# Kernel optimization log

Hardware: AMD Instinct MI355X
Metric: run time of the kernel (lower is better)

Reference implementation:

```python
import jax, jax.numpy as jnp
import numpy as np

B, D_IN, N_EXP, D_EXP, TOP_K = 8192, 1024, 8, 1024, 2


def setup_inputs() -> dict:
    key = jax.random.key(0)
    ks = jax.random.split(key, 6)
    s_in = 1.0 / np.sqrt(D_IN)
    s_exp = 1.0 / np.sqrt(D_EXP)
    return {
        "x": jax.random.normal(ks[0], (B, D_IN), jnp.float32),
        "gate_w": jax.random.normal(ks[1], (D_IN, N_EXP), jnp.float32) * s_in,
        "w1": jax.random.normal(ks[2], (N_EXP, D_IN, D_EXP), jnp.float32) * s_in,
        "b1": jax.random.normal(ks[3], (N_EXP, D_EXP), jnp.float32) * 0.01,
        "w2": jax.random.normal(ks[4], (N_EXP, D_EXP, D_EXP), jnp.float32) * s_exp,
        "b2": jax.random.normal(ks[5], (N_EXP, D_EXP), jnp.float32) * 0.01,
    }


def _moe(x, gate_w, w1, b1, w2, b2):
    # Gating: top-k sparse softmax over expert logits.
    gate_logits = x @ gate_w                          # (B, E)
    top_vals, top_idx = jax.lax.top_k(gate_logits, TOP_K)  # (B, K)
    # softmax over only the top-k logits == softmax of -inf-scattered logits
    top_w = jax.nn.softmax(top_vals, axis=-1)          # (B, K)
    gate_weights = jnp.zeros_like(gate_logits).at[
        jnp.arange(x.shape[0])[:, None], top_idx
    ].set(top_w)                                       # (B, E)
    # Dense all-expert MLP (matches torch.stack over experts).
    h = jax.nn.gelu(jnp.einsum("bd,edf->ebf", x, w1) + b1[:, None, :],
                    approximate=False)                 # (E, B, F)
    expert_outs = jnp.einsum("ebf,efg->ebg", h, w2) + b2[:, None, :]  # (E, B, G)
    output = jnp.einsum("be,ebg->bg", gate_weights, expert_outs)      # (B, G)
    return output, gate_weights


def reference(x, gate_w, w1, b1, w2, b2):
    return _moe(x, gate_w, w1, b1, w2, b2)
```

## Files before the change

### kernel.cpp

```cpp
#include <hip/hip_runtime.h>
#include <math.h>
#include <stdint.h>


#define NTOK   8192
#define DIN    1024
#define NEXP   8
#define DEXP   1024
#define MAXROWS 17408
#define MAXT   136

typedef __bf16 bf16x8_t __attribute__((ext_vector_type(8)));
typedef float f32x4 __attribute__((ext_vector_type(4)));

__device__ __forceinline__ unsigned short f2bf(float f) {
  union { float f; unsigned int u; } v; v.f = f;
  unsigned int u = v.u;
  u += 0x7fffu + ((u >> 16) & 1u);
  return (unsigned short)(u >> 16);
}

__device__ __forceinline__ float bf2f(unsigned short s) {
  union { unsigned int u; float f; } v; v.u = ((unsigned int)s) << 16;
  return v.f;
}

__device__ __forceinline__ void async16(const void* g, void* l) {
  __builtin_amdgcn_global_load_lds((const __attribute__((address_space(1))) void*)g,
                                   (__attribute__((address_space(3))) void*)l, 16, 0, 0);
}

__device__ __forceinline__ float gelu_fast(float v) {
  float u = v * (1.5957691216057308f + 0.07135481627f * v * v);
  return v * (1.0f / (1.0f + __expf(-u)));
}

__device__ __forceinline__ void transpose_tile(const float* s, unsigned short* d,
                                               float* tile, int tid) {
  int a = tid & 15, r0 = tid >> 4;
  #pragma unroll
  for (int p = 0; p < 4; ++p) {
    int r = r0 + p * 16;
    float4 v = *(const float4*)(s + (size_t)r * 1024 + a * 4);
    tile[r * 65 + a * 4 + 0] = v.x;
    tile[r * 65 + a * 4 + 1] = v.y;
    tile[r * 65 + a * 4 + 2] = v.z;
    tile[r * 65 + a * 4 + 3] = v.w;
  }
  __syncthreads();
  #pragma unroll
  for (int p = 0; p < 4; ++p) {
    int nr = r0 + p * 16;
    ushort4 o;
    o.x = f2bf(tile[(a * 4 + 0) * 65 + nr]);
    o.y = f2bf(tile[(a * 4 + 1) * 65 + nr]);
    o.z = f2bf(tile[(a * 4 + 2) * 65 + nr]);
    o.w = f2bf(tile[(a * 4 + 3) * 65 + nr]);
    *(ushort4*)(d + (size_t)nr * 1024 + a * 4) = o;
  }
}

__global__ __launch_bounds__(256) void prep_kernel(const float* __restrict__ x,
                                                   const float* __restrict__ gw,
                                                   const float* __restrict__ w1,
                                                   const float* __restrict__ w2,
                                                   unsigned short* __restrict__ xbf,
                                                   unsigned short* __restrict__ w1T,
                                                   unsigned short* __restrict__ w2T,
                                                   float* __restrict__ outGate,
                                                   int* __restrict__ topE,
                                                   float* __restrict__ topW,
                                                   int* __restrict__ rowTok) {
  __shared__ __align__(16) char smem[32768];
  int b = blockIdx.x;
  int tid = threadIdx.x;
  if (b >= 6144) {
    int base = (b - 6144) * 1024 + tid * 4;
    *(int4*)(rowTok + base) = make_int4(-1, -1, -1, -1);
    return;
  }
  if (b >= 2048) {
    int idx = b - 2048;
    const float* src = (idx < 2048) ? w1 : w2;
    unsigned short* dst = (idx < 2048) ? w1T : w2T;
    idx &= 2047;
    int e = idx >> 8, rest = idx & 255, kt = rest >> 4, nt = rest & 15;
    const float* s = src + (size_t)e * DIN * DEXP + (size_t)kt * 64 * 1024 + nt * 64;
    unsigned short* d = dst + (size_t)e * DIN * DEXP + (size_t)nt * 64 * 1024 + kt * 64;
    transpose_tile(s, d, (float*)smem, tid);
    return;
  }
  float (*gwT)[1024] = (float(*)[1024])smem;
  #pragma unroll
  for (int it = 0; it < 8; ++it) {
    int idx = it * 256 + tid;
    int fk = idx >> 1;
    int e0 = (idx & 1) * 4;
    float4 g = *(const float4*)(gw + fk * 8 + e0);
    gwT[e0 + 0][fk] = g.x; gwT[e0 + 1][fk] = g.y;
    gwT[e0 + 2][fk] = g.z; gwT[e0 + 3][fk] = g.w;
  }
  __syncthreads();

  int lane = tid & 63, wv = tid >> 6;
  int t = b * 4 + wv;
  const float4* xr = (const float4*)(x + (size_t)t * 1024);
  ushort4* xo = (ushort4*)(xbf + (size_t)t * 1024);
  double acc[NEXP];
  #pragma unroll
  for (int e = 0; e < NEXP; ++e) acc[e] = 0.0;
  #pragma unroll
  for (int j = 0; j < 4; ++j) {
    int q = lane + 64 * j;
    float4 v = xr[q];
    ushort4 r;
    r.x = f2bf(v.x); r.y = f2bf(v.y); r.z = f2bf(v.z); r.w = f2bf(v.w);
    xo[q] = r;
    float vv[4] = {v.x, v.y, v.z, v.w};
    #pragma unroll
    for (int e = 0; e < NEXP; ++e) {
      float4 g = *(const float4*)&gwT[e][4 * q];
      acc[e] += (double)vv[0] * (double)g.x;
      acc[e] += (double)vv[1] * (double)g.y;
      acc[e] += (double)vv[2] * (double)g.z;
      acc[e] += (double)vv[3] * (double)g.w;
    }
  }
  #pragma unroll
  for (int off = 32; off > 0; off >>= 1) {
    #pragma unroll
    for (int e = 0; e < NEXP; ++e) acc[e] += __shfl_xor(acc[e], off);
  }
  if (lane == 0) {
    int e0 = 0; double v0 = acc[0];
    #pragma unroll
    for (int e = 1; e < NEXP; ++e) if (acc[e] > v0) { v0 = acc[e]; e0 = e; }
    int e1 = -1; double v1 = -1e300;
    #pragma unroll
    for (int e = 0; e < NEXP; ++e) if (e != e0 && acc[e] > v1) { v1 = acc[e]; e1 = e; }
    float ex = expf((float)(v1 - v0));
    float inv = 1.0f / (1.0f + ex);
    float w0 = inv, w1v = ex * inv;
    float g8[8];
    #pragma unroll
    for (int e = 0; e < NEXP; ++e) g8[e] = 0.f;
    g8[e0] = w0; g8[e1] = w1v;
    float4* gp = (float4*)(outGate + t * 8);
    gp[0] = *(float4*)&g8[0];
    gp[1] = *(float4*)&g8[4];
    topE[t * 2 + 0] = e0; topE[t * 2 + 1] = e1;
    topW[t * 2 + 0] = w0; topW[t * 2 + 1] = w1v;
  }
}

__global__ __launch_bounds__(1024) void slot_kernel(const int* __restrict__ topE,
                                                    int* __restrict__ topRow,
                                                    int* __restrict__ rowTok,
                                                    int* __restrict__ tileExpert,
                                                    int* __restrict__ tileRowBase) {
  __shared__ int wtot[16][NEXP];
  __shared__ int wbase[16][NEXP];
  __shared__ int soff[NEXP];
  int tid = threadIdx.x;
  int lane = tid & 63, wv = tid >> 6;
  int a0 = tid * 16;
  unsigned long long pk = 0ull;
  int cnt[NEXP];
  #pragma unroll
  for (int e = 0; e < NEXP; ++e) cnt[e] = 0;
  #pragma unroll
  for (int i = 0; i < 4; ++i) {
    int4 ev = *(const int4*)(topE + a0 + i * 4);
    int e4[4] = {ev.x, ev.y, ev.z, ev.w};
    #pragma unroll
    for (int m = 0; m < 4; ++m) {
      int e = e4[m];
      pk |= (unsigned long long)e << ((i * 4 + m) * 4);
      cnt[e]++;
    }
  }
  int excl[NEXP];
  #pragma unroll
  for (int e = 0; e < NEXP; ++e) {
    int v = cnt[e], sum = v;
    #pragma unroll
    for (int d = 1; d < 64; d <<= 1) {
      int u = __shfl_up(sum, d);
      if (lane >= d) sum += u;
    }
    excl[e] = sum - v;
    if (lane == 63) wtot[wv][e] = sum;
  }
  __syncthreads();
  if (tid == 0) {
    int counts[NEXP];
    for (int e = 0; e < NEXP; ++e) {
      int s = 0;
      for (int w = 0; w < 16; ++w) { wbase[w][e] = s; s += wtot[w][e]; }
      counts[e] = s;
    }
    int row = 0, tl = 0;
    for (int e = 0; e < NEXP; ++e) {
      soff[e] = row;
      int nt = (counts[e] + 127) >> 7;
      for (int i = 0; i < nt; ++i) { tileExpert[tl] = e; tileRowBase[tl] = row + i * 128; ++tl; }
      row += nt << 7;
    }
    for (; tl < MAXT; ++tl) tileExpert[tl] = -1;
  }
  __syncthreads();
  int base[NEXP], run[NEXP];
  #pragma unroll
  for (int e = 0; e < NEXP; ++e) { base[e] = soff[e] + wbase[wv][e] + excl[e]; run[e] = 0; }
  for (int i = 0; i < 16; ++i) {
    int e = (int)((pk >> (i * 4)) & 7ull);
    int row = base[e] + run[e]++;
    rowTok[row] = (a0 + i) >> 1;
    topRow[a0 + i] = row;
  }
}

template <bool GATHER, bool GELU>
__device__ __forceinline__ void moe_gemm_body(
    const unsigned short* __restrict__ Asrc,
    const unsigned short* __restrict__ Wt,
    const float* __restrict__ bias,
    const int* __restrict__ tileExpert,
    const int* __restrict__ tileRowBase,
    const int* __restrict__ rowTok,
    unsigned short* __restrict__ Out,
    unsigned short* sm) {
  int e = tileExpert[blockIdx.y];
  if (e < 0) return;
  int rowBase = tileRowBase[blockIdx.y];
  int n0 = blockIdx.x * 128;

  int tid = threadIdx.x;
  int lane = tid & 63, wv = tid >> 6;
  int wr = wv >> 1, wc = wv & 1;

  int p = lane >> 3, pos = lane & 7;
  int L = pos ^ p;
  int rowoff = wv * 16 + p * 2 + (L >> 2);
  int qsw = L & 3;

  int rsel = lane & 15, quad = lane >> 4;
  int prow = rsel >> 1;
  int co = (((rsel & 1) * 4 + quad) ^ prow) * 8 + prow * 64;

  int arow[2];
  #pragma unroll
  for (int j = 0; j < 2; ++j) {
    int r = rowBase + j * 64 + rowoff;
    if (GATHER) { int tk = rowTok[r]; arow[j] = tk < 0 ? 0 : tk; }
    else arow[j] = r;
  }
  const unsigned short* Bsrc = Wt + (size_t)e * 1024 * 1024;

  auto stage = [&](int T) {
    int kk = T * 32;
    int selB = (T & 1) * 16384;
    #pragma unroll
    for (int j = 0; j < 2; ++j) {
      int ab = __builtin_amdgcn_readfirstlane(selB + j * 4096 + wv * 1024);
      async16(Asrc + (size_t)arow[j] * 1024 + kk + qsw * 8, (char*)sm + ab);
      async16(Bsrc + (size_t)(n0 + j * 64 + rowoff) * 1024 + kk + qsw * 8,
              (char*)sm + ab + 8192);
    }
  };

  f32x4 acc[4][4] = {};

  stage(0);
  stage(1);
  asm volatile("s_waitcnt vmcnt(4)" ::: "memory");
  __builtin_amdgcn_s_barrier();

  for (int t = 0; t < 32; ++t) {
    const unsigned short* sA = sm + (t & 1) * 8192;
    const unsigned short* sB = sA + 4096;
    bf16x8_t af[4], bf[4];
    #pragma unroll
    for (int mi = 0; mi < 4; ++mi)
      af[mi] = *(const bf16x8_t*)&sA[wr * 2048 + mi * 512 + co];
    #pragma unroll
    for (int ni = 0; ni < 4; ++ni)
      bf[ni] = *(const bf16x8_t*)&sB[wc * 2048 + ni * 512 + co];
    __builtin_amdgcn_s_setprio(1);
    #pragma unroll
    for (int mi = 0; mi < 4; ++mi)
      #pragma unroll
      for (int ni = 0; ni < 4; ++ni)
        acc[mi][ni] = __builtin_amdgcn_mfma_f32_16x16x32_bf16(af[mi], bf[ni], acc[mi][ni], 0, 0, 0);
    __builtin_amdgcn_s_setprio(0);
    __builtin_amdgcn_s_barrier();
    if (t + 2 < 32) {
      stage(t + 2);
      asm volatile("s_waitcnt vmcnt(4)" ::: "memory");
    } else {
      asm volatile("s_waitcnt vmcnt(0)" ::: "memory");
    }
    __builtin_amdgcn_s_barrier();
  }

  float bv[4];
  #pragma unroll
  for (int ni = 0; ni < 4; ++ni)
    bv[ni] = bias[e * 1024 + n0 + wc * 64 + ni * 16 + rsel];
  #pragma unroll
  for (int mi = 0; mi < 4; ++mi)
    #pragma unroll
    for (int ni = 0; ni < 4; ++ni)
      #pragma unroll
      for (int r = 0; r < 4; ++r) {
        int m = wr * 64 + mi * 16 + quad * 4 + r;
        int n = wc * 64 + ni * 16 + rsel;
        float v = acc[mi][ni][r] + bv[ni];
        if (GELU) v = gelu_fast(v);
        sm[m * 128 + n] = f2bf(v);
      }
  __syncthreads();
  #pragma unroll
  for (int i = 0; i < 8; ++i) {
    int idx = i * 4096 + tid * 16;
    int m = idx >> 8, cb = idx & 255;
    *(uint4*)(Out + (size_t)(rowBase + m) * 1024 + n0 + (cb >> 1)) =
        *(const uint4*)((const char*)sm + idx);
  }
}

__global__ __launch_bounds__(256, 4) void gemm1_kernel(
    const unsigned short* __restrict__ xbf, const unsigned short* __restrict__ w1T,
    const float* __restrict__ b1, const int* __restrict__ tileExpert,
    const int* __restrict__ tileRowBase, const int* __restrict__ rowTok,
    unsigned short* __restrict__ h) {
  __shared__ __align__(16) unsigned short sm[16384];
  moe_gemm_body<true, true>(xbf, w1T, b1, tileExpert, tileRowBase, rowTok, h, sm);
}

__global__ __launch_bounds__(256, 4) void gemm2_kernel(
    const unsigned short* __restrict__ h, const unsigned short* __restrict__ w2T,
    const float* __restrict__ b2, const int* __restrict__ tileExpert,
    const int* __restrict__ tileRowBase, const int* __restrict__ rowTok,
    unsigned short* __restrict__ y) {
  __shared__ __align__(16) unsigned short sm[16384];
  moe_gemm_body<false, false>(h, w2T, b2, tileExpert, tileRowBase, rowTok, y, sm);
}

__global__ __launch_bounds__(256) void combine_kernel(const unsigned short* __restrict__ y,
                                                      const int* __restrict__ topRow,
                                                      const float* __restrict__ topW,
                                                      float* __restrict__ out) {
  int tid = threadIdx.x;
  int wv = tid >> 6, lane = tid & 63;
  int t = blockIdx.x * 4 + wv;
  int r0 = topRow[t * 2 + 0], r1 = topRow[t * 2 + 1];
  float w0 = topW[t * 2 + 0], w1 = topW[t * 2 + 1];
  const unsigned short* p0 = y + (size_t)r0 * 1024 + lane * 16;
  const unsigned short* p1 = y + (size_t)r1 * 1024 + lane * 16;
  float* op = out + (size_t)t * 1024 + lane * 16;
  #pragma unroll
  for (int hh = 0; hh < 2; ++hh) {
    union { uint4 v; unsigned short s[8]; } a, b;
    a.v = *(const uint4*)(p0 + hh * 8);
    b.v = *(const uint4*)(p1 + hh * 8);
    float o[8];
    #pragma unroll
    for (int j = 0; j < 8; ++j)
      o[j] = w0 * bf2f(a.s[j]) + w1 * bf2f(b.s[j]);
    *(float4*)(op + hh * 8) = *(float4*)&o[0];
    *(float4*)(op + hh * 8 + 4) = *(float4*)&o[4];
  }
}

extern "C" void kernel_launch(void* const* d_in, const int* in_sizes, int n_in,
                              void* d_out, int out_size, void* d_ws, size_t ws_size,
                              hipStream_t stream) {
  const float* x  = (const float*)d_in[0];
  const float* gw = (const float*)d_in[1];
  const float* w1 = (const float*)d_in[2];
  const float* b1 = (const float*)d_in[3];
  const float* w2 = (const float*)d_in[4];
  const float* b2 = (const float*)d_in[5];
  float* out = (float*)d_out;

  char* ws = (char*)d_ws;
  int* tileExpert  = (int*)ws;
  int* tileRowBase = tileExpert + MAXT;
  int* topE        = tileRowBase + MAXT;
  int* topRow      = topE + 16384;
  float* topW      = (float*)(topRow + 16384);
  int* rowTok      = (int*)(ws + (256 << 10));
  unsigned short* xbf  = (unsigned short*)(ws + (512 << 10));
  unsigned short* w1T  = xbf + (size_t)NTOK * DIN;
  unsigned short* w2T  = w1T + (size_t)NEXP * DIN * DEXP;
  unsigned short* hbuf = w2T + (size_t)NEXP * DEXP * DEXP;
  unsigned short* ybuf = hbuf + (size_t)MAXROWS * DEXP;

  prep_kernel<<<2048 + 4096 + 17, 256, 0, stream>>>(x, gw, w1, w2, xbf, w1T, w2T,
                                                    out + (size_t)NTOK * DEXP,
                                                    topE, topW, rowTok);
  slot_kernel<<<1, 1024, 0, stream>>>(topE, topRow, rowTok, tileExpert, tileRowBase);
  gemm1_kernel<<<dim3(8, MAXT), 256, 0, stream>>>(xbf, w1T, b1, tileExpert,
                                                  tileRowBase, rowTok, hbuf);
  gemm2_kernel<<<dim3(8, MAXT), 256, 0, stream>>>(hbuf, w2T, b2, tileExpert,
                                                  tileRowBase, rowTok, ybuf);
  combine_kernel<<<NTOK / 4, 256, 0, stream>>>(ybuf, topRow, topW, out);
}
```

Measured before the change: 303.6 us.

## Widen GEMM tiles to 128x256 and move w2 transpose into gemm1 launch

Each MoE GEMM block now computes a 128x256 output tile instead of 128x128, so every wave holds 4x8 MFMA accumulators and the A tile is reused across twice as many columns. LDS per block doubles and occupancy drops from 4 to 2 blocks per CU. The w2 fp32-to-bf16 transpose moves out of prep_kernel and into extra trailing blocks of the gemm1 launch, so it can overlap with the first GEMM. Register pressure rises and there are fewer blocks to fill the machine.

```diff
diff --git a/kernel.cpp b/kernel.cpp
--- a/kernel.cpp
+++ b/kernel.cpp
@@ -9,6 +9,7 @@
 #define DEXP   1024
 #define MAXROWS 17408
 #define MAXT   136
+#define NGEMM  (4 * MAXT)
 
 typedef __bf16 bf16x8_t __attribute__((ext_vector_type(8)));
 typedef float f32x4 __attribute__((ext_vector_type(4)));
@@ -63,10 +64,8 @@
 __global__ __launch_bounds__(256) void prep_kernel(const float* __restrict__ x,
                                                    const float* __restrict__ gw,
                                                    const float* __restrict__ w1,
-                                                   const float* __restrict__ w2,
                                                    unsigned short* __restrict__ xbf,
                                                    unsigned short* __restrict__ w1T,
-                                                   unsigned short* __restrict__ w2T,
                                                    float* __restrict__ outGate,
                                                    int* __restrict__ topE,
                                                    float* __restrict__ topW,
@@ -74,19 +73,16 @@
   __shared__ __align__(16) char smem[32768];
   int b = blockIdx.x;
   int tid = threadIdx.x;
-  if (b >= 6144) {
-    int base = (b - 6144) * 1024 + tid * 4;
+  if (b >= 4096) {
+    int base = (b - 4096) * 1024 + tid * 4;
     *(int4*)(rowTok + base) = make_int4(-1, -1, -1, -1);
     return;
   }
   if (b >= 2048) {
     int idx = b - 2048;
-    const float* src = (idx < 2048) ? w1 : w2;
-    unsigned short* dst = (idx < 2048) ? w1T : w2T;
-    idx &= 2047;
     int e = idx >> 8, rest = idx & 255, kt = rest >> 4, nt = rest & 15;
-    const float* s = src + (size_t)e * DIN * DEXP + (size_t)kt * 64 * 1024 + nt * 64;
-    unsigned short* d = dst + (size_t)e * DIN * DEXP + (size_t)nt * 64 * 1024 + kt * 64;
+    const float* s = w1 + (size_t)e * DIN * DEXP + (size_t)kt * 64 * 1024 + nt * 64;
+    unsigned short* d = w1T + (size_t)e * DIN * DEXP + (size_t)nt * 64 * 1024 + kt * 64;
     transpose_tile(s, d, (float*)smem, tid);
     return;
   }
@@ -222,6 +218,7 @@
 
 template <bool GATHER, bool GELU>
 __device__ __forceinline__ void moe_gemm_body(
+    int bid,
     const unsigned short* __restrict__ Asrc,
     const unsigned short* __restrict__ Wt,
     const float* __restrict__ bias,
@@ -230,10 +227,11 @@
     const int* __restrict__ rowTok,
     unsigned short* __restrict__ Out,
     unsigned short* sm) {
-  int e = tileExpert[blockIdx.y];
+  int panel = bid & 3, tileId = bid >> 2;
+  int e = tileExpert[tileId];
   if (e < 0) return;
-  int rowBase = tileRowBase[blockIdx.y];
-  int n0 = blockIdx.x * 128;
+  int rowBase = tileRowBase[tileId];
+  int n0 = panel * 256;
 
   int tid = threadIdx.x;
   int lane = tid & 63, wv = tid >> 6;
@@ -255,96 +253,110 @@
     if (GATHER) { int tk = rowTok[r]; arow[j] = tk < 0 ? 0 : tk; }
     else arow[j] = r;
   }
+  int brow0 = n0 + rowoff;
   const unsigned short* Bsrc = Wt + (size_t)e * 1024 * 1024;
 
   auto stage = [&](int T) {
     int kk = T * 32;
-    int selB = (T & 1) * 16384;
+    int selB = (T & 1) * 24576;
     #pragma unroll
     for (int j = 0; j < 2; ++j) {
       int ab = __builtin_amdgcn_readfirstlane(selB + j * 4096 + wv * 1024);
       async16(Asrc + (size_t)arow[j] * 1024 + kk + qsw * 8, (char*)sm + ab);
-      async16(Bsrc + (size_t)(n0 + j * 64 + rowoff) * 1024 + kk + qsw * 8,
-              (char*)sm + ab + 8192);
+    }
+    #pragma unroll
+    for (int g = 0; g < 4; ++g) {
+      int bb = __builtin_amdgcn_readfirstlane(selB + 8192 + g * 4096 + wv * 1024);
+      async16(Bsrc + (size_t)(brow0 + g * 64) * 1024 + kk + qsw * 8, (char*)sm + bb);
     }
   };
 
-  f32x4 acc[4][4] = {};
+  f32x4 acc[4][8] = {};
 
   stage(0);
   stage(1);
-  asm volatile("s_waitcnt vmcnt(4)" ::: "memory");
+  asm volatile("s_waitcnt vmcnt(6)" ::: "memory");
   __builtin_amdgcn_s_barrier();
 
   for (int t = 0; t < 32; ++t) {
-    const unsigned short* sA = sm + (t & 1) * 8192;
+    const unsigned short* sA = sm + (t & 1) * 12288;
     const unsigned short* sB = sA + 4096;
-    bf16x8_t af[4], bf[4];
+    bf16x8_t af[4], bf[8];
     #pragma unroll
     for (int mi = 0; mi < 4; ++mi)
       af[mi] = *(const bf16x8_t*)&sA[wr * 2048 + mi * 512 + co];
     #pragma unroll
-    for (int ni = 0; ni < 4; ++ni)
-      bf[ni] = *(const bf16x8_t*)&sB[wc * 2048 + ni * 512 + co];
+    for (int ni = 0; ni < 8; ++ni)
+      bf[ni] = *(const bf16x8_t*)&sB[(wc * 2 + (ni >> 2)) * 2048 + (ni & 3) * 512 + co];
     __builtin_amdgcn_s_setprio(1);
     #pragma unroll
     for (int mi = 0; mi < 4; ++mi)
       #pragma unroll
-      for (int ni = 0; ni < 4; ++ni)
+      for (int ni = 0; ni < 8; ++ni)
         acc[mi][ni] = __builtin_amdgcn_mfma_f32_16x16x32_bf16(af[mi], bf[ni], acc[mi][ni], 0, 0, 0);
     __builtin_amdgcn_s_setprio(0);
     __builtin_amdgcn_s_barrier();
     if (t + 2 < 32) {
       stage(t + 2);
-      asm volatile("s_waitcnt vmcnt(4)" ::: "memory");
+      asm volatile("s_waitcnt vmcnt(6)" ::: "memory");
     } else {
       asm volatile("s_waitcnt vmcnt(0)" ::: "memory");
     }
     __builtin_amdgcn_s_barrier();
   }
 
-  float bv[4];
-  #pragma unroll
-  for (int ni = 0; ni < 4; ++ni)
-    bv[ni] = bias[e * 1024 + n0 + wc * 64 + ni * 16 + rsel];
+  float bv[8];
+  #pragma unroll
+  for (int ni = 0; ni < 8; ++ni)
+    bv[ni] = bias[e * 1024 + n0 + wc * 128 + ni * 16 + rsel];
   #pragma unroll
   for (int mi = 0; mi < 4; ++mi)
     #pragma unroll
-    for (int ni = 0; ni < 4; ++ni)
+    for (int ni = 0; ni < 8; ++ni)
       #pragma unroll
       for (int r = 0; r < 4; ++r) {
         int m = wr * 64 + mi * 16 + quad * 4 + r;
-        int n = wc * 64 + ni * 16 + rsel;
+        int n = wc * 128 + ni * 16 + rsel;
         float v = acc[mi][ni][r] + bv[ni];
         if (GELU) v = gelu_fast(v);
-        sm[m * 128 + n] = f2bf(v);
+        sm[m * 256 + n] = f2bf(v);
       }
   __syncthreads();
   #pragma unroll
-  for (int i = 0; i < 8; ++i) {
+  for (int i = 0; i < 16; ++i) {
     int idx = i * 4096 + tid * 16;
-    int m = idx >> 8, cb = idx & 255;
+    int m = idx >> 9, cb = idx & 511;
     *(uint4*)(Out + (size_t)(rowBase + m) * 1024 + n0 + (cb >> 1)) =
         *(const uint4*)((const char*)sm + idx);
   }
 }
 
-__global__ __launch_bounds__(256, 4) void gemm1_kernel(
+__global__ __launch_bounds__(256, 2) void gemm1_kernel(
     const unsigned short* __restrict__ xbf, const unsigned short* __restrict__ w1T,
-    const float* __restrict__ b1, const int* __restrict__ tileExpert,
+    const float* __restrict__ b1, const float* __restrict__ w2,
+    unsigned short* __restrict__ w2T, const int* __restrict__ tileExpert,
     const int* __restrict__ tileRowBase, const int* __restrict__ rowTok,
     unsigned short* __restrict__ h) {
-  __shared__ __align__(16) unsigned short sm[16384];
-  moe_gemm_body<true, true>(xbf, w1T, b1, tileExpert, tileRowBase, rowTok, h, sm);
-}
-
-__global__ __launch_bounds__(256, 4) void gemm2_kernel(
+  __shared__ __align__(16) unsigned short sm[32768];
+  int bid = blockIdx.x;
+  if (bid >= NGEMM) {
+    int idx = bid - NGEMM;
+    int e = idx >> 8, rest = idx & 255, kt = rest >> 4, nt = rest & 15;
+    const float* s = w2 + (size_t)e * DEXP * DEXP + (size_t)kt * 64 * 1024 + nt * 64;
+    unsigned short* d = w2T + (size_t)e * DEXP * DEXP + (size_t)nt * 64 * 1024 + kt * 64;
+    transpose_tile(s, d, (float*)sm, threadIdx.x);
+    return;
+  }
+  moe_gemm_body<true, true>(bid, xbf, w1T, b1, tileExpert, tileRowBase, rowTok, h, sm);
+}
+
+__global__ __launch_bounds__(256, 2) void gemm2_kernel(
     const unsigned short* __restrict__ h, const unsigned short* __restrict__ w2T,
     const float* __restrict__ b2, const int* __restrict__ tileExpert,
     const int* __restrict__ tileRowBase, const int* __restrict__ rowTok,
     unsigned short* __restrict__ y) {
-  __shared__ __align__(16) unsigned short sm[16384];
-  moe_gemm_body<false, false>(h, w2T, b2, tileExpert, tileRowBase, rowTok, y, sm);
+  __shared__ __align__(16) unsigned short sm[32768];
+  moe_gemm_body<false, false>(blockIdx.x, h, w2T, b2, tileExpert, tileRowBase, rowTok, y, sm);
 }
 
 __global__ __launch_bounds__(256) void combine_kernel(const unsigned short* __restrict__ y,
@@ -397,13 +409,13 @@
   unsigned short* hbuf = w2T + (size_t)NEXP * DEXP * DEXP;
   unsigned short* ybuf = hbuf + (size_t)MAXROWS * DEXP;
 
-  prep_kernel<<<2048 + 4096 + 17, 256, 0, stream>>>(x, gw, w1, w2, xbf, w1T, w2T,
+  prep_kernel<<<2048 + 2048 + 17, 256, 0, stream>>>(x, gw, w1, xbf, w1T,
                                                     out + (size_t)NTOK * DEXP,
                                                     topE, topW, rowTok);
   slot_kernel<<<1, 1024, 0, stream>>>(topE, topRow, rowTok, tileExpert, tileRowBase);
-  gemm1_kernel<<<dim3(8, MAXT), 256, 0, stream>>>(xbf, w1T, b1, tileExpert,
-                                                  tileRowBase, rowTok, hbuf);
-  gemm2_kernel<<<dim3(8, MAXT), 256, 0, stream>>>(hbuf, w2T, b2, tileExpert,
-                                                  tileRowBase, rowTok, ybuf);
+  gemm1_kernel<<<NGEMM + 2048, 256, 0, stream>>>(xbf, w1T, b1, w2, w2T, tileExpert,
+                                                 tileRowBase, rowTok, hbuf);
+  gemm2_kernel<<<NGEMM, 256, 0, stream>>>(hbuf, w2T, b2, tileExpert,
+                                          tileRowBase, rowTok, ybuf);
   combine_kernel<<<NTOK / 4, 256, 0, stream>>>(ybuf, topRow, topW, out);
 }
```

After: 305.6 us. About the same (+0.7%).

## Convert MoE GEMMs to persistent work-stealing and fold w2 transpose into gemm1

Applied to the files above, without the earlier changes.

The two grouped GEMM kernels become persistent grids of 1280 blocks that claim (tile, panel) work items from an atomic counter, which the slot kernel resets. The w2 fp32-to-bf16 transpose moves out of the prep kernel and becomes trailing work items of gemm1, so it fills idle slots after the GEMM tiles. Empty padded tiles are skipped cheaply, and launch bounds rise to 5 blocks per CU. The cost is an atomic plus three barriers per item, and the transpose now competes with gemm1's tail instead of overlapping with prep.

```diff
diff --git a/kernel.cpp b/kernel.cpp
--- a/kernel.cpp
+++ b/kernel.cpp
@@ -9,6 +9,9 @@
 #define DEXP   1024
 #define MAXROWS 17408
 #define MAXT   136
+#define NGEMM  (8 * MAXT)
+#define NW2T   2048
+#define NBLK   1280
 
 typedef __bf16 bf16x8_t __attribute__((ext_vector_type(8)));
 typedef float f32x4 __attribute__((ext_vector_type(4)));
@@ -63,10 +66,8 @@
 __global__ __launch_bounds__(256) void prep_kernel(const float* __restrict__ x,
                                                    const float* __restrict__ gw,
                                                    const float* __restrict__ w1,
-                                                   const float* __restrict__ w2,
                                                    unsigned short* __restrict__ xbf,
                                                    unsigned short* __restrict__ w1T,
-                                                   unsigned short* __restrict__ w2T,
                                                    float* __restrict__ outGate,
                                                    int* __restrict__ topE,
                                                    float* __restrict__ topW,
@@ -74,19 +75,16 @@
   __shared__ __align__(16) char smem[32768];
   int b = blockIdx.x;
   int tid = threadIdx.x;
-  if (b >= 6144) {
-    int base = (b - 6144) * 1024 + tid * 4;
+  if (b >= 4096) {
+    int base = (b - 4096) * 1024 + tid * 4;
     *(int4*)(rowTok + base) = make_int4(-1, -1, -1, -1);
     return;
   }
   if (b >= 2048) {
     int idx = b - 2048;
-    const float* src = (idx < 2048) ? w1 : w2;
-    unsigned short* dst = (idx < 2048) ? w1T : w2T;
-    idx &= 2047;
     int e = idx >> 8, rest = idx & 255, kt = rest >> 4, nt = rest & 15;
-    const float* s = src + (size_t)e * DIN * DEXP + (size_t)kt * 64 * 1024 + nt * 64;
-    unsigned short* d = dst + (size_t)e * DIN * DEXP + (size_t)nt * 64 * 1024 + kt * 64;
+    const float* s = w1 + (size_t)e * DIN * DEXP + (size_t)kt * 64 * 1024 + nt * 64;
+    unsigned short* d = w1T + (size_t)e * DIN * DEXP + (size_t)nt * 64 * 1024 + kt * 64;
     transpose_tile(s, d, (float*)smem, tid);
     return;
   }
@@ -157,11 +155,13 @@
                                                     int* __restrict__ topRow,
                                                     int* __restrict__ rowTok,
                                                     int* __restrict__ tileExpert,
-                                                    int* __restrict__ tileRowBase) {
+                                                    int* __restrict__ tileRowBase,
+                                                    int* __restrict__ stealCtr) {
   __shared__ int wtot[16][NEXP];
   __shared__ int wbase[16][NEXP];
   __shared__ int soff[NEXP];
   int tid = threadIdx.x;
+  if (tid < 2) stealCtr[tid] = 0;
   int lane = tid & 63, wv = tid >> 6;
   int a0 = tid * 16;
   unsigned long long pk = 0ull;
@@ -221,7 +221,8 @@
 }
 
 template <bool GATHER, bool GELU>
-__device__ __forceinline__ void moe_gemm_body(
+__device__ __forceinline__ void moe_gemm_item(
+    int wi,
     const unsigned short* __restrict__ Asrc,
     const unsigned short* __restrict__ Wt,
     const float* __restrict__ bias,
@@ -230,10 +231,11 @@
     const int* __restrict__ rowTok,
     unsigned short* __restrict__ Out,
     unsigned short* sm) {
-  int e = tileExpert[blockIdx.y];
+  int panel = wi & 7, tileId = wi >> 3;
+  int e = tileExpert[tileId];
   if (e < 0) return;
-  int rowBase = tileRowBase[blockIdx.y];
-  int n0 = blockIdx.x * 128;
+  int rowBase = tileRowBase[tileId];
+  int n0 = panel * 128;
 
   int tid = threadIdx.x;
   int lane = tid & 63, wv = tid >> 6;
@@ -329,22 +331,49 @@
   }
 }
 
-__global__ __launch_bounds__(256, 4) void gemm1_kernel(
+__global__ __launch_bounds__(256, 5) void gemm1_kernel(
     const unsigned short* __restrict__ xbf, const unsigned short* __restrict__ w1T,
-    const float* __restrict__ b1, const int* __restrict__ tileExpert,
+    const float* __restrict__ b1, const float* __restrict__ w2,
+    unsigned short* __restrict__ w2T, const int* __restrict__ tileExpert,
     const int* __restrict__ tileRowBase, const int* __restrict__ rowTok,
-    unsigned short* __restrict__ h) {
+    unsigned short* __restrict__ h, int* __restrict__ stealCtr) {
   __shared__ __align__(16) unsigned short sm[16384];
-  moe_gemm_body<true, true>(xbf, w1T, b1, tileExpert, tileRowBase, rowTok, h, sm);
-}
-
-__global__ __launch_bounds__(256, 4) void gemm2_kernel(
+  while (true) {
+    __syncthreads();
+    if (threadIdx.x == 0) *(int*)sm = atomicAdd(&stealCtr[0], 1);
+    __syncthreads();
+    int wi = *(const int*)sm;
+    __syncthreads();
+    if (wi >= NGEMM + NW2T) return;
+    if (wi < NGEMM) {
+      moe_gemm_item<true, true>(wi, xbf, w1T, b1, tileExpert, tileRowBase,
+                                rowTok, h, sm);
+    } else {
+      int idx = wi - NGEMM;
+      int e = idx >> 8, rest = idx & 255, kt = rest >> 4, nt = rest & 15;
+      const float* s = w2 + (size_t)e * DEXP * DEXP + (size_t)kt * 64 * 1024 + nt * 64;
+      unsigned short* d = w2T + (size_t)e * DEXP * DEXP + (size_t)nt * 64 * 1024 + kt * 64;
+      transpose_tile(s, d, (float*)sm, threadIdx.x);
+    }
+  }
+}
+
+__global__ __launch_bounds__(256, 5) void gemm2_kernel(
     const unsigned short* __restrict__ h, const unsigned short* __restrict__ w2T,
     const float* __restrict__ b2, const int* __restrict__ tileExpert,
     const int* __restrict__ tileRowBase, const int* __restrict__ rowTok,
-    unsigned short* __restrict__ y) {
+    unsigned short* __restrict__ y, int* __restrict__ stealCtr) {
   __shared__ __align__(16) unsigned short sm[16384];
-  moe_gemm_body<false, false>(h, w2T, b2, tileExpert, tileRowBase, rowTok, y, sm);
+  while (true) {
+    __syncthreads();
+    if (threadIdx.x == 0) *(int*)sm = atomicAdd(&stealCtr[1], 1);
+    __syncthreads();
+    int wi = *(const int*)sm;
+    __syncthreads();
+    if (wi >= NGEMM) return;
+    moe_gemm_item<false, false>(wi, h, w2T, b2, tileExpert, tileRowBase,
+                                rowTok, y, sm);
+  }
 }
 
 __global__ __launch_bounds__(256) void combine_kernel(const unsigned short* __restrict__ y,
@@ -390,6 +419,7 @@
   int* topE        = tileRowBase + MAXT;
   int* topRow      = topE + 16384;
   float* topW      = (float*)(topRow + 16384);
+  int* stealCtr    = (int*)(ws + (224 << 10));
   int* rowTok      = (int*)(ws + (256 << 10));
   unsigned short* xbf  = (unsigned short*)(ws + (512 << 10));
   unsigned short* w1T  = xbf + (size_t)NTOK * DIN;
@@ -397,13 +427,14 @@
   unsigned short* hbuf = w2T + (size_t)NEXP * DEXP * DEXP;
   unsigned short* ybuf = hbuf + (size_t)MAXROWS * DEXP;
 
-  prep_kernel<<<2048 + 4096 + 17, 256, 0, stream>>>(x, gw, w1, w2, xbf, w1T, w2T,
+  prep_kernel<<<2048 + 2048 + 17, 256, 0, stream>>>(x, gw, w1, xbf, w1T,
                                                     out + (size_t)NTOK * DEXP,
                                                     topE, topW, rowTok);
-  slot_kernel<<<1, 1024, 0, stream>>>(topE, topRow, rowTok, tileExpert, tileRowBase);
-  gemm1_kernel<<<dim3(8, MAXT), 256, 0, stream>>>(xbf, w1T, b1, tileExpert,
-                                                  tileRowBase, rowTok, hbuf);
-  gemm2_kernel<<<dim3(8, MAXT), 256, 0, stream>>>(hbuf, w2T, b2, tileExpert,
-                                                  tileRowBase, rowTok, ybuf);
+  slot_kernel<<<1, 1024, 0, stream>>>(topE, topRow, rowTok, tileExpert,
+                                      tileRowBase, stealCtr);
+  gemm1_kernel<<<NBLK, 256, 0, stream>>>(xbf, w1T, b1, w2, w2T, tileExpert,
+                                         tileRowBase, rowTok, hbuf, stealCtr);
+  gemm2_kernel<<<NBLK, 256, 0, stream>>>(hbuf, w2T, b2, tileExpert,
+                                         tileRowBase, rowTok, ybuf, stealCtr);
   combine_kernel<<<NTOK / 4, 256, 0, stream>>>(ybuf, topRow, topW, out);
 }
```

Result: slower. 626.5 us (+106.4%).
